# Kernel optimization log

Hardware: AMD Instinct MI355X
Metric: run time of the kernel (lower is better)

Reference implementation:

```python
import jax, jax.numpy as jnp
import numpy as np

B, T, L, M = 64, 2000, 400, 80
SIGMA_FACTOR = 0.05
SIGMA_CAP = 10.0
SIGMA_MIN = 1.5
WARMUP_STEPS = 10000
GLOBAL_STEP = 0  # fresh loss module -> progress = 0
ENTROPY_TARGET = 3.5
ATTN_W_START = 1.0
ATTN_W_MIN = 0.2
EPS = 1e-8


def setup_inputs() -> dict:
    key = jax.random.key(0)
    ks = jax.random.split(key, 8)
    mel_out_postnet = jax.random.normal(ks[0], (B, T, M), jnp.float32)
    mel_out = jax.random.normal(ks[1], (B, T, M), jnp.float32)
    gate_out = jax.random.normal(ks[2], (B, T), jnp.float32)
    # alignments: stacked per-step attention, row-normalized like real softmax outputs
    a = jax.random.uniform(ks[3], (B, T, L), jnp.float32)
    alignments = a / jnp.sum(a, axis=-1, keepdims=True)
    mel_target = jax.random.normal(ks[4], (B, T, M), jnp.float32)
    gate_target = jnp.round(jax.random.uniform(ks[5], (B, T), jnp.float32))
    mel_lengths = jax.random.randint(ks[6], (B,), T // 2, T + 1, jnp.int32).at[0].set(T)
    text_lengths = jax.random.randint(ks[7], (B,), L // 2, L + 1, jnp.int32).at[0].set(L)
    return {
        "mel_out_postnet": mel_out_postnet, "mel_out": mel_out, "gate_out": gate_out,
        "alignments": alignments, "mel_target": mel_target, "gate_target": gate_target,
        "mel_lengths": mel_lengths, "text_lengths": text_lengths,
    }


def _diagonal_target(text_lengths):
    # sigma per batch element; global_step=0 -> progress=0 -> sigma = init_sigma
    init_sigma = jnp.clip(text_lengths.astype(jnp.float32) * SIGMA_FACTOR, 3.0, SIGMA_CAP)
    progress = min(1.0, GLOBAL_STEP / float(WARMUP_STEPS))
    sigma = init_sigma - (init_sigma - SIGMA_MIN) * progress  # [B]
    t = jnp.arange(T, dtype=jnp.int32)  # decoder steps
    Lb = text_lengths[:, None]  # [B,1]
    # expected_pos = min(int(t*Lb/T), Lb-1); positive ints -> integer floor div matches trunc
    exp_pos = jnp.minimum((t[None, :] * Lb) // T, Lb - 1).astype(jnp.float32)  # [B,T]
    pos = jnp.arange(L, dtype=jnp.float32)  # [L]
    z = (pos[None, None, :] - exp_pos[:, :, None]) / sigma[:, None, None]
    g = jnp.exp(-0.5 * z * z)  # [B,T,L]
    valid = (pos[None, None, :] < text_lengths[:, None, None].astype(jnp.float32))
    g = g * valid
    return g / (jnp.sum(g, axis=-1, keepdims=True) + EPS)


def reference(mel_out_postnet, mel_out, gate_out, alignments, mel_target,
              gate_target, mel_lengths, text_lengths):
    # masked L1 on mel (mel_target already [B,T,M], matching the torch transpose)
    valid = (jnp.arange(T)[None, :] < mel_lengths[:, None])[:, :, None]  # [B,T,1]
    vf = valid.astype(jnp.float32)
    n_valid = jnp.sum(vf) * M
    mel_loss_1 = jnp.sum(jnp.abs(mel_out - mel_target) * vf) / n_valid
    mel_loss_2 = jnp.sum(jnp.abs(mel_out_postnet - mel_target) * vf) / n_valid
    loss_mel = mel_loss_1 + mel_loss_2

    # BCEWithLogits, mean reduction (stable form)
    x, z_t = gate_out, gate_target
    loss_gate = jnp.mean(jnp.maximum(x, 0.0) - x * z_t + jnp.log1p(jnp.exp(-jnp.abs(x))))

    # guided-attention KL against diagonal Gaussian target
    target = _diagonal_target(text_lengths)  # [B,T,L]
    attn_safe = jnp.maximum(alignments, EPS)
    log_pred = jnp.log(attn_safe)
    kl_pw = jnp.where(target > 0.0, target * (jnp.log(jnp.maximum(target, EPS)) - log_pred), 0.0)
    attention_kl = jnp.sum(kl_pw) / B / T  # batchmean then / T_dec
    attention_kl = jnp.minimum(attention_kl, 150.0)

    # entropy-gated attention weight (python-float in torch -> stop_gradient)
    attn_entropy = jnp.mean(-jnp.sum(attn_safe * log_pred, axis=2))
    ratio = jnp.maximum(attn_entropy / ENTROPY_TARGET, 0.0)
    weight = jnp.where(attn_entropy <= ENTROPY_TARGET,
                       jnp.maximum(ATTN_W_MIN, ATTN_W_START * ratio),
                       ATTN_W_START)
    weight = jax.lax.stop_gradient(weight)

    total_loss = loss_mel + loss_gate + weight * attention_kl
    return (total_loss, loss_mel, loss_gate, attention_kl)
```

## Files before the change

kernel.cpp:

```cpp
#include <hip/hip_runtime.h>
#include <cstddef>
#include <cstdint>

#define B_ 64
#define T_ 2000
#define L_ 400
#define M_ 80
#define EPSF 1e-8f
#define LOG_EPSF -18.420680743952367f

#define NBLK 2048
#define TBL_N (B_ * L_)

__device__ inline float waveReduce(float v) {
#pragma unroll
  for (int m = 32; m >= 1; m >>= 1) v += __shfl_xor(v, m, 64);
  return v;
}

__global__ __launch_bounds__(256) void table_kernel(
    const int* __restrict__ text_lengths, float4* __restrict__ tbl) {
  const int lane = threadIdx.x & 63;
  const int wid = (blockIdx.x * 256 + threadIdx.x) >> 6;
  if (wid >= TBL_N) return;
  const int b = wid / L_;
  const int epi = wid - b * L_;
  const int Lb = text_lengths[b];
  const float sigma = fminf(fmaxf((float)Lb * 0.05f, 3.0f), 10.0f);
  const float invsig = 1.0f / sigma;
  const float epf = (float)epi;
  float S = 0.f;
#pragma unroll
  for (int k = 0; k < 7; ++k) {
    int l = lane + 64 * k;
    if (l < Lb) {
      float z = ((float)l - epf) * invsig;
      S += __expf(-0.5f * z * z);
    }
  }
  S = waveReduce(S);
  if (lane == 0) {
    float Se = S + EPSF;
    float4 e;
    e.x = 1.0f / Se;
    e.y = __logf(Se);
    e.z = invsig;
    e.w = epf;
    tbl[wid] = e;
  }
}

__global__ __launch_bounds__(256) void fused_kernel(
    const float4* __restrict__ mo, const float4* __restrict__ mp,
    const float4* __restrict__ mt, const float4* __restrict__ gx,
    const float4* __restrict__ gz, const float4* __restrict__ align4,
    const float4* __restrict__ tbl,
    const int* __restrict__ mel_lengths, const int* __restrict__ text_lengths,
    double* __restrict__ partials) {
  const int tid = blockIdx.x * 256 + threadIdx.x;
  const int nthreads = NBLK * 256;

  float mel_acc = 0.f;
  const int N4 = B_ * T_ * (M_ / 4);
  for (int i = tid; i < N4; i += nthreads) {
    int row = i / (M_ / 4);
    int b = row / T_;
    int t = row - b * T_;
    if (t < mel_lengths[b]) {
      float4 a = mo[i], c = mp[i], d = mt[i];
      mel_acc += fabsf(a.x - d.x) + fabsf(a.y - d.y) + fabsf(a.z - d.z) + fabsf(a.w - d.w)
               + fabsf(c.x - d.x) + fabsf(c.y - d.y) + fabsf(c.z - d.z) + fabsf(c.w - d.w);
    }
  }

  float gate_acc = 0.f;
  for (int i = tid; i < (B_ * T_) / 4; i += nthreads) {
    float4 xv = gx[i], zv = gz[i];
    gate_acc += fmaxf(xv.x, 0.f) - xv.x * zv.x + log1pf(__expf(-fabsf(xv.x)))
              + fmaxf(xv.y, 0.f) - xv.y * zv.y + log1pf(__expf(-fabsf(xv.y)))
              + fmaxf(xv.z, 0.f) - xv.z * zv.z + log1pf(__expf(-fabsf(xv.z)))
              + fmaxf(xv.w, 0.f) - xv.w * zv.w + log1pf(__expf(-fabsf(xv.w)));
  }

  float kl_acc = 0.f, ent_acc = 0.f;
  const int NA4 = B_ * T_ * (L_ / 4);
  for (int i = tid; i < NA4; i += nthreads) {
    int row = i / (L_ / 4);
    int li4 = i - row * (L_ / 4);
    int l0 = li4 * 4;
    int b = row / T_;
    int t = row - b * T_;
    int Lb = text_lengths[b];
    int epi = t * Lb / T_;
    int lim = Lb - 1;
    if (epi > lim) epi = lim;
    float4 tb = tbl[b * L_ + epi];
    float4 a4 = align4[i];
    float av[4] = {a4.x, a4.y, a4.z, a4.w};
#pragma unroll
    for (int j = 0; j < 4; ++j) {
      float as = fmaxf(av[j], EPSF);
      float lp = __logf(as);
      ent_acc -= as * lp;
      int l = l0 + j;
      if (l < Lb) {
        float z = ((float)l - tb.w) * tb.z;
        float e = -0.5f * z * z;
        float tgt = __expf(e) * tb.x;
        float lt = fmaxf(e - tb.y, LOG_EPSF);
        kl_acc += tgt * (lt - lp);
      }
    }
  }

  float w0 = waveReduce(mel_acc);
  float w1 = waveReduce(gate_acc);
  float w2 = waveReduce(kl_acc);
  float w3 = waveReduce(ent_acc);
  __shared__ double sh[4][4];
  const int lane = threadIdx.x & 63, wib = threadIdx.x >> 6;
  if (lane == 0) {
    sh[wib][0] = (double)w0; sh[wib][1] = (double)w1;
    sh[wib][2] = (double)w2; sh[wib][3] = (double)w3;
  }
  __syncthreads();
  if (threadIdx.x == 0) {
    partials[blockIdx.x]            = sh[0][0] + sh[1][0] + sh[2][0] + sh[3][0];
    partials[NBLK + blockIdx.x]     = sh[0][1] + sh[1][1] + sh[2][1] + sh[3][1];
    partials[2 * NBLK + blockIdx.x] = sh[0][2] + sh[1][2] + sh[2][2] + sh[3][2];
    partials[3 * NBLK + blockIdx.x] = sh[0][3] + sh[1][3] + sh[2][3] + sh[3][3];
  }
}

__device__ double segSum(const double* __restrict__ p, int n, double* sh) {
  double a = 0.0;
  for (int i = threadIdx.x; i < n; i += 256) a += p[i];
  sh[threadIdx.x] = a;
  __syncthreads();
  for (int s = 128; s > 0; s >>= 1) {
    if ((int)threadIdx.x < s) sh[threadIdx.x] += sh[threadIdx.x + s];
    __syncthreads();
  }
  double r = sh[0];
  __syncthreads();
  return r;
}

__global__ __launch_bounds__(256) void finalize_kernel(
    const double* __restrict__ partials, const int* __restrict__ mel_lengths,
    float* __restrict__ out) {
  __shared__ double sh[256];
  double mel_sum  = segSum(partials, NBLK, sh);
  double gate_sum = segSum(partials + NBLK, NBLK, sh);
  double kl_sum   = segSum(partials + 2 * NBLK, NBLK, sh);
  double ent_sum  = segSum(partials + 3 * NBLK, NBLK, sh);
  if (threadIdx.x == 0) {
    long nv = 0;
    for (int b = 0; b < B_; ++b) nv += mel_lengths[b];
    double n_valid = (double)nv * (double)M_;
    float loss_mel  = (float)(mel_sum / n_valid);
    float loss_gate = (float)(gate_sum / (double)(B_ * T_));
    float kl  = (float)(kl_sum / (double)(B_ * T_));
    kl = fminf(kl, 150.0f);
    float ent = (float)(ent_sum / (double)(B_ * T_));
    float ratio = fmaxf(ent / 3.5f, 0.0f);
    float weight = (ent <= 3.5f) ? fmaxf(0.2f, 1.0f * ratio) : 1.0f;
    out[0] = loss_mel + loss_gate + weight * kl;
    out[1] = loss_mel;
    out[2] = loss_gate;
    out[3] = kl;
  }
}

extern "C" void kernel_launch(void* const* d_in, const int* in_sizes, int n_in,
                              void* d_out, int out_size, void* d_ws, size_t ws_size,
                              hipStream_t stream) {
  const float* mel_out_postnet = (const float*)d_in[0];
  const float* mel_out         = (const float*)d_in[1];
  const float* gate_out        = (const float*)d_in[2];
  const float* alignments      = (const float*)d_in[3];
  const float* mel_target      = (const float*)d_in[4];
  const float* gate_target     = (const float*)d_in[5];
  const int*   mel_lengths     = (const int*)d_in[6];
  const int*   text_lengths    = (const int*)d_in[7];
  float* out = (float*)d_out;

  float4* tbl = (float4*)d_ws;
  double* partials = (double*)((char*)d_ws + TBL_N * sizeof(float4));

  table_kernel<<<dim3((TBL_N * 64 + 255) / 256), dim3(256), 0, stream>>>(
      text_lengths, tbl);
  fused_kernel<<<dim3(NBLK), dim3(256), 0, stream>>>(
      (const float4*)mel_out, (const float4*)mel_out_postnet,
      (const float4*)mel_target, (const float4*)gate_out,
      (const float4*)gate_target, (const float4*)alignments, tbl,
      mel_lengths, text_lengths, partials);
  finalize_kernel<<<dim3(1), dim3(256), 0, stream>>>(partials, mel_lengths, out);
}
```

Measured before the change: 398.6 us.

## Precompute per-row target table and process 64 rows per block with batched loads

Adds an expand kernel that writes one packed per-row entry holding the normalizer, log normalizer, inverse sigma, expected position, text length and mel-valid flag. This removes the per-element integer divisions and the indirect table lookups from the main loop. The fused kernel now gives each block a fixed run of 64 rows across alignments, mel and gate, and issues 5 independent float4 loads per group to expose memory-level parallelism. The cost is an extra launch plus about 2 MB of workspace traffic for the row table.

Result: no change. 395.9 us (-0.7%).

```diff
diff --git a/kernel.cpp b/kernel.cpp
--- a/kernel.cpp
+++ b/kernel.cpp
@@ -9,8 +9,9 @@
 #define EPSF 1e-8f
 #define LOG_EPSF -18.420680743952367f
 
-#define NBLK 2048
 #define TBL_N (B_ * L_)
+#define NROW (B_ * T_)
+#define NBLK 2000
 
 __device__ inline float waveReduce(float v) {
 #pragma unroll
@@ -41,76 +42,105 @@
   S = waveReduce(S);
   if (lane == 0) {
     float Se = S + EPSF;
-    float4 e;
-    e.x = 1.0f / Se;
-    e.y = __logf(Se);
-    e.z = invsig;
-    e.w = epf;
-    tbl[wid] = e;
-  }
+    tbl[wid] = make_float4(1.0f / Se, __logf(Se), invsig, 0.f);
+  }
+}
+
+__global__ __launch_bounds__(256) void expand_kernel(
+    const float4* __restrict__ tbl, const int* __restrict__ text_lengths,
+    const int* __restrict__ mel_lengths, float4* __restrict__ rowtbl) {
+  int p = blockIdx.x * 256 + threadIdx.x;
+  if (p >= NROW) return;
+  int b = p / T_;
+  int t = p - b * T_;
+  int Lb = text_lengths[b];
+  int epi = t * Lb / T_;
+  if (epi > Lb - 1) epi = Lb - 1;
+  float4 e = tbl[b * L_ + epi];
+  int melv = (t < mel_lengths[b]) ? 1 : 0;
+  int w = epi | (Lb << 10) | (melv << 19);
+  rowtbl[p] = make_float4(e.x, e.y, e.z, (float)w);
 }
 
 __global__ __launch_bounds__(256) void fused_kernel(
     const float4* __restrict__ mo, const float4* __restrict__ mp,
     const float4* __restrict__ mt, const float4* __restrict__ gx,
     const float4* __restrict__ gz, const float4* __restrict__ align4,
-    const float4* __restrict__ tbl,
-    const int* __restrict__ mel_lengths, const int* __restrict__ text_lengths,
-    double* __restrict__ partials) {
-  const int tid = blockIdx.x * 256 + threadIdx.x;
-  const int nthreads = NBLK * 256;
-
-  float mel_acc = 0.f;
-  const int N4 = B_ * T_ * (M_ / 4);
-  for (int i = tid; i < N4; i += nthreads) {
-    int row = i / (M_ / 4);
-    int b = row / T_;
-    int t = row - b * T_;
-    if (t < mel_lengths[b]) {
-      float4 a = mo[i], c = mp[i], d = mt[i];
-      mel_acc += fabsf(a.x - d.x) + fabsf(a.y - d.y) + fabsf(a.z - d.z) + fabsf(a.w - d.w)
-               + fabsf(c.x - d.x) + fabsf(c.y - d.y) + fabsf(c.z - d.z) + fabsf(c.w - d.w);
-    }
-  }
-
-  float gate_acc = 0.f;
-  for (int i = tid; i < (B_ * T_) / 4; i += nthreads) {
-    float4 xv = gx[i], zv = gz[i];
-    gate_acc += fmaxf(xv.x, 0.f) - xv.x * zv.x + log1pf(__expf(-fabsf(xv.x)))
-              + fmaxf(xv.y, 0.f) - xv.y * zv.y + log1pf(__expf(-fabsf(xv.y)))
-              + fmaxf(xv.z, 0.f) - xv.z * zv.z + log1pf(__expf(-fabsf(xv.z)))
-              + fmaxf(xv.w, 0.f) - xv.w * zv.w + log1pf(__expf(-fabsf(xv.w)));
-  }
-
-  float kl_acc = 0.f, ent_acc = 0.f;
-  const int NA4 = B_ * T_ * (L_ / 4);
-  for (int i = tid; i < NA4; i += nthreads) {
-    int row = i / (L_ / 4);
-    int li4 = i - row * (L_ / 4);
-    int l0 = li4 * 4;
-    int b = row / T_;
-    int t = row - b * T_;
-    int Lb = text_lengths[b];
-    int epi = t * Lb / T_;
-    int lim = Lb - 1;
-    if (epi > lim) epi = lim;
-    float4 tb = tbl[b * L_ + epi];
-    float4 a4 = align4[i];
-    float av[4] = {a4.x, a4.y, a4.z, a4.w};
-#pragma unroll
-    for (int j = 0; j < 4; ++j) {
-      float as = fmaxf(av[j], EPSF);
-      float lp = __logf(as);
-      ent_acc -= as * lp;
-      int l = l0 + j;
-      if (l < Lb) {
-        float z = ((float)l - tb.w) * tb.z;
-        float e = -0.5f * z * z;
-        float tgt = __expf(e) * tb.x;
-        float lt = fmaxf(e - tb.y, LOG_EPSF);
-        kl_acc += tgt * (lt - lp);
+    const float4* __restrict__ rowtbl, double* __restrict__ partials) {
+  const int tid = threadIdx.x;
+  const int base_row = blockIdx.x * 64;
+  float mel_acc = 0.f, gate_acc = 0.f, kl_acc = 0.f, ent_acc = 0.f;
+
+  const float4* __restrict__ ab = align4 + (size_t)base_row * (L_ / 4);
+  const float4* __restrict__ rt = rowtbl + base_row;
+  for (int kk = 0; kk < 5; ++kk) {
+    float4 a[5], tb[5];
+    int l0[5];
+#pragma unroll
+    for (int j = 0; j < 5; ++j) {
+      int idx = tid + 256 * (kk * 5 + j);
+      unsigned r = (unsigned)idx / 100u;
+      a[j] = ab[idx];
+      tb[j] = rt[r];
+      l0[j] = (idx - (int)r * 100) * 4;
+    }
+#pragma unroll
+    for (int j = 0; j < 5; ++j) {
+      int wi = (int)tb[j].w;
+      float epf = (float)(wi & 1023);
+      int Lb = (wi >> 10) & 511;
+      float inv = tb[j].x, logSe = tb[j].y, invsig = tb[j].z;
+      float av[4] = {a[j].x, a[j].y, a[j].z, a[j].w};
+#pragma unroll
+      for (int q = 0; q < 4; ++q) {
+        float as = fmaxf(av[q], EPSF);
+        float lp = __logf(as);
+        ent_acc -= as * lp;
+        int l = l0[j] + q;
+        if (l < Lb) {
+          float z = ((float)l - epf) * invsig;
+          float e = -0.5f * z * z;
+          float tgt = __expf(e) * inv;
+          float lt = fmaxf(e - logSe, LOG_EPSF);
+          kl_acc += tgt * (lt - lp);
+        }
       }
     }
+  }
+
+  {
+    const float4* __restrict__ mob = mo + (size_t)base_row * (M_ / 4);
+    const float4* __restrict__ mpb = mp + (size_t)base_row * (M_ / 4);
+    const float4* __restrict__ mtb = mt + (size_t)base_row * (M_ / 4);
+    float4 A[5], C[5], D[5];
+    int mv[5];
+#pragma unroll
+    for (int j = 0; j < 5; ++j) {
+      int idx = tid + 256 * j;
+      unsigned r = (unsigned)idx / 20u;
+      A[j] = mob[idx];
+      C[j] = mpb[idx];
+      D[j] = mtb[idx];
+      mv[j] = ((int)rt[r].w) >> 19;
+    }
+#pragma unroll
+    for (int j = 0; j < 5; ++j) {
+      if (mv[j]) {
+        mel_acc += fabsf(A[j].x - D[j].x) + fabsf(A[j].y - D[j].y)
+                 + fabsf(A[j].z - D[j].z) + fabsf(A[j].w - D[j].w)
+                 + fabsf(C[j].x - D[j].x) + fabsf(C[j].y - D[j].y)
+                 + fabsf(C[j].z - D[j].z) + fabsf(C[j].w - D[j].w);
+      }
+    }
+  }
+
+  if (tid < 16) {
+    float4 xv = gx[base_row / 4 + tid];
+    float4 zv = gz[base_row / 4 + tid];
+    gate_acc = fmaxf(xv.x, 0.f) - xv.x * zv.x + log1pf(__expf(-fabsf(xv.x)))
+             + fmaxf(xv.y, 0.f) - xv.y * zv.y + log1pf(__expf(-fabsf(xv.y)))
+             + fmaxf(xv.z, 0.f) - xv.z * zv.z + log1pf(__expf(-fabsf(xv.z)))
+             + fmaxf(xv.w, 0.f) - xv.w * zv.w + log1pf(__expf(-fabsf(xv.w)));
   }
 
   float w0 = waveReduce(mel_acc);
@@ -124,7 +154,7 @@
     sh[wib][2] = (double)w2; sh[wib][3] = (double)w3;
   }
   __syncthreads();
-  if (threadIdx.x == 0) {
+  if (tid == 0) {
     partials[blockIdx.x]            = sh[0][0] + sh[1][0] + sh[2][0] + sh[3][0];
     partials[NBLK + blockIdx.x]     = sh[0][1] + sh[1][1] + sh[2][1] + sh[3][1];
     partials[2 * NBLK + blockIdx.x] = sh[0][2] + sh[1][2] + sh[2][2] + sh[3][2];
@@ -186,14 +216,17 @@
   float* out = (float*)d_out;
 
   float4* tbl = (float4*)d_ws;
-  double* partials = (double*)((char*)d_ws + TBL_N * sizeof(float4));
+  float4* rowtbl = (float4*)((char*)d_ws + (size_t)TBL_N * 16);
+  double* partials = (double*)((char*)d_ws + (size_t)(TBL_N + NROW) * 16);
 
   table_kernel<<<dim3((TBL_N * 64 + 255) / 256), dim3(256), 0, stream>>>(
       text_lengths, tbl);
+  expand_kernel<<<dim3((NROW + 255) / 256), dim3(256), 0, stream>>>(
+      tbl, text_lengths, mel_lengths, rowtbl);
   fused_kernel<<<dim3(NBLK), dim3(256), 0, stream>>>(
       (const float4*)mel_out, (const float4*)mel_out_postnet,
       (const float4*)mel_target, (const float4*)gate_out,
-      (const float4*)gate_target, (const float4*)alignments, tbl,
-      mel_lengths, text_lengths, partials);
+      (const float4*)gate_target, (const float4*)alignments,
+      rowtbl, partials);
   finalize_kernel<<<dim3(1), dim3(256), 0, stream>>>(partials, mel_lengths, out);
 }
```
